# Performance work log

Measured on AMD Instinct MI355X. Metric: run time of the kernel, lower is better.

The kernel has to match this reference:

```python
import jax, jax.numpy as jnp
import numpy as np


def pairwise_euclidean_distance(x, y):
    # x: [N, D], y: [K, D] -> [N, K] squared Euclidean distances
    cross = -2.0 * (x @ y.T)
    x_term = jnp.sum(x * x, axis=1, keepdims=True)      # [N, 1]
    y_term = jnp.sum(y * y, axis=1, keepdims=True).T    # [1, K]
    return cross + x_term + y_term


def quantize(z, centroids):
    # z: [B, T, D], centroids: [K, D]
    B, T, D = z.shape
    flat = z.reshape(-1, D)                              # [N, D]
    distances = pairwise_euclidean_distance(flat, centroids)
    alignment = jnp.argmin(distances, axis=1)            # [N]
    q = centroids[alignment]                             # gather [N, D]
    # straight-through estimator: grad flows to z, not centroids
    q = flat + jax.lax.stop_gradient(q - flat)
    return q.reshape(B, T, D)


def setup_inputs() -> dict:
    key = jax.random.key(0)
    ks = jax.random.split(key, 5)
    B, T, F, D, K = 16, 2048, 80, 512, 2048
    return {
        "x": jax.random.normal(ks[0], (B, T, F), dtype=jnp.float32),
        "W_enc": jax.random.normal(ks[1], (F, D), dtype=jnp.float32) * (1.0 / np.sqrt(F)),
        "b_enc": jnp.zeros((D,), dtype=jnp.float32),
        "centroids": jax.random.normal(ks[2], (K, D), dtype=jnp.float32),
        "W_dec": jax.random.normal(ks[3], (D, F), dtype=jnp.float32) * (1.0 / np.sqrt(D)),
        "b_dec": jnp.zeros((F,), dtype=jnp.float32),
    }


def reference(x, W_enc, b_enc, centroids, W_dec, b_dec):
    z = x @ W_enc + b_enc            # encoder: [B, T, D]
    zq = quantize(z, centroids)      # VQ: distance + argmin + gather
    out = zq @ W_dec + b_dec         # decoder: [B, T, F]
    return out
```

## Files before the change

kernel.cpp:

```cpp
#include <hip/hip_runtime.h>
#include <hip/hip_bf16.h>

#define N_TOK  32768
#define F_IN   80
#define D_DIM  512
#define K_CENT 2048
#define F_OUT  80
#define TM     16
#define KP     96
#define M2     0.5f
#define QSLOTS 12
#define QREC   104
#define TREC   416
#define JTOT   160

typedef __attribute__((ext_vector_type(8)))  short bf16x8;
typedef __attribute__((ext_vector_type(4)))  float fx4;
typedef __attribute__((ext_vector_type(16))) float fx16;

#define AS3 __attribute__((address_space(3)))
#define AS1 __attribute__((address_space(1)))

__device__ inline unsigned short f2bf(float f) {
    unsigned u = __float_as_uint(f);
    return (unsigned short)((u + 0x7FFFu + ((u >> 16) & 1u)) >> 16);
}
__device__ inline float bf2f(unsigned short h) {
    return __uint_as_float((unsigned)h << 16);
}

__device__ inline void gll16(const unsigned short* g, unsigned short* l) {
    __builtin_amdgcn_global_load_lds((const AS1 unsigned*)g, (AS3 unsigned*)l, 16, 0, 0);
}

__device__ inline unsigned fkey(float f) {
    unsigned b = __float_as_uint(f);
    return b ^ ((b >> 31) ? 0xFFFFFFFFu : 0x80000000u);
}
__device__ inline float keyf(unsigned k) {
    unsigned b = k ^ ((k & 0x80000000u) ? 0x80000000u : 0xFFFFFFFFu);
    return __uint_as_float(b);
}

__device__ inline size_t frag32_addr(int row, int k) {
    int sub = (row >> 5) * 2 + ((k >> 4) & 1);
    int L = (row & 31) + ((k >> 3) & 1) * 32;
    return (size_t)sub * 512 + L * 8 + (k & 7);
}

__global__ __launch_bounds__(256) void k_prep1(
    const float* __restrict__ x, const float* __restrict__ Wenc,
    const float* __restrict__ Wdec,
    unsigned short* __restrict__ xbt, float* __restrict__ Bcat) {
    const int bid = blockIdx.x, tid = threadIdx.x;
    if (bid < 1536) {
        int o = bid * 256 + tid;
        int m = o / 12;
        int ko = (o - m * 12) * 8;
        unsigned short u[8];
        if (ko < F_IN) {
            const float* src = x + (size_t)m * F_IN + ko;
            float4 v0 = *(const float4*)src;
            float4 v1 = *(const float4*)(src + 4);
            u[0]=f2bf(v0.x); u[1]=f2bf(v0.y); u[2]=f2bf(v0.z); u[3]=f2bf(v0.w);
            u[4]=f2bf(v1.x); u[5]=f2bf(v1.y); u[6]=f2bf(v1.z); u[7]=f2bf(v1.w);
        } else if (ko == 80) {
            u[0] = 0x3F80; u[1] = 0x3F80;
#pragma unroll
            for (int j = 2; j < 8; ++j) u[j] = 0;
        } else {
#pragma unroll
            for (int j = 0; j < 8; ++j) u[j] = 0;
        }
        int mt = m >> 7, kt = ko >> 5, row = m & 127, kl = ko & 31;
        uint4 p;
        p.x = (unsigned)u[0] | ((unsigned)u[1] << 16);
        p.y = (unsigned)u[2] | ((unsigned)u[3] << 16);
        p.z = (unsigned)u[4] | ((unsigned)u[5] << 16);
        p.w = (unsigned)u[6] | ((unsigned)u[7] << 16);
        *(uint4*)&xbt[(size_t)(mt * 3 + kt) * 4096 + frag32_addr(row, kl)] = p;
    } else {
        int e = (bid - 1536) * 256 + tid;
        int d = e / JTOT, j = e - d * JTOT;
        float v = (j < F_OUT) ? Wdec[(size_t)d * F_OUT + j]
                              : Wenc[(size_t)(j - F_OUT) * D_DIM + d];
        Bcat[e] = v;
    }
}

__global__ void k_cadjf2(const float* __restrict__ cent, const float* __restrict__ benc,
                         float* __restrict__ cnorm, unsigned short* __restrict__ Gbt) {
    int wave = threadIdx.x >> 6, lane = threadIdx.x & 63;
    int k = blockIdx.x * 4 + wave;
    const float* row = cent + (size_t)k * D_DIM;
    float s = 0.f, t = 0.f;
#pragma unroll
    for (int j = 0; j < 8; ++j) {
        float c = row[lane + 64 * j];
        float b = benc[lane + 64 * j];
        s += c * c; t += b * c;
    }
#pragma unroll
    for (int off = 32; off; off >>= 1) { s += __shfl_down(s, off); t += __shfl_down(t, off); }
    const int nt = k >> 7, cl = k & 127;
    const size_t tb = (size_t)(nt * 3 + 2) * 4096;
    if (lane < 14)
        Gbt[tb + frag32_addr(cl, 18 + lane)] = 0;
    if (lane == 0) {
        cnorm[k] = s;
        float v = -0.5f * (s - 2.0f * t);
        unsigned short h = f2bf(v);
        unsigned short l = f2bf(v - bf2f(h));
        Gbt[tb + frag32_addr(cl, 16)] = h;
        Gbt[tb + frag32_addr(cl, 17)] = l;
    }
}

__global__ __launch_bounds__(192) void k_cgemm(
    const float* __restrict__ cent, const float* __restrict__ Bcat,
    const float* __restrict__ bdec, unsigned short* __restrict__ Gbt,
    float* __restrict__ dec) {
    const int j = threadIdx.x;
    if (j >= JTOT) return;
    const int k0 = blockIdx.x * 4;
    const float* c0 = cent + (size_t)k0 * D_DIM;
    float a0 = 0.f, a1 = 0.f, a2 = 0.f, a3 = 0.f;
#pragma unroll 4
    for (int d = 0; d < D_DIM; ++d) {
        float b  = Bcat[d * JTOT + j];
        float v0 = c0[d];
        float v1 = c0[D_DIM + d];
        float v2 = c0[2 * D_DIM + d];
        float v3 = c0[3 * D_DIM + d];
        a0 += v0 * b; a1 += v1 * b; a2 += v2 * b; a3 += v3 * b;
    }
    float a[4] = { a0, a1, a2, a3 };
    if (j < F_OUT) {
        float bd = bdec[j];
#pragma unroll
        for (int c = 0; c < 4; ++c)
            dec[(size_t)(k0 + c) * F_OUT + j] = a[c] + bd;
    } else {
        int f = j - F_OUT;
#pragma unroll
        for (int c = 0; c < 4; ++c) {
            int k = k0 + c;
            Gbt[(size_t)((k >> 7) * 3 + (f >> 5)) * 4096 + frag32_addr(k & 127, f & 31)]
                = f2bf(a[c]);
        }
    }
}

__global__ __launch_bounds__(512) void k_dist3(
    const unsigned short* __restrict__ xbt, const unsigned short* __restrict__ Gbt,
    char* __restrict__ lists) {
    __shared__ unsigned short Bs[2][12288];
    __shared__ int cnt[128];
    __shared__ unsigned mxk[128];

    const int tid = threadIdx.x;
    const int bid = blockIdx.x;
    const int mt = bid >> 2, nq = bid & 3;
    const int lane = tid & 63;
    const int wave = tid >> 6;
    const int tg = wave >> 1;
    const int ch = wave & 1;
    const int col = lane & 31;
    const int hi = lane >> 5;

    if (tid < 128) { cnt[tid] = 0; mxk[tid] = 0u; }

    bf16x8 bfr[6];
    const unsigned short* Ab = xbt + (size_t)mt * 12288;
#pragma unroll
    for (int kc = 0; kc < 6; ++kc)
        bfr[kc] = *(const bf16x8*)&Ab[(kc >> 1) * 4096 + (tg * 2 + (kc & 1)) * 512 + lane * 8];

    const int woff = (tid & ~63) * 8;
    const unsigned short* Gq = Gbt + (size_t)nq * 4 * 12288;
#pragma unroll
    for (int q = 0; q < 3; ++q)
        gll16(Gq + q * 4096 + tid * 8, &Bs[0][0] + q * 4096 + woff);

    float rmax = -3.4e38f;
    int cur = 0;
    for (int t4 = 0; t4 < 4; ++t4) {
        __syncthreads();
        if (t4 + 1 < 4) {
#pragma unroll
            for (int q = 0; q < 3; ++q)
                gll16(Gq + (size_t)(t4 + 1) * 12288 + q * 4096 + tid * 8,
                      &Bs[cur ^ 1][0] + q * 4096 + woff);
        }
        const unsigned short* B = &Bs[cur][0];
        fx16 acc[2];
#pragma unroll
        for (int u = 0; u < 2; ++u)
#pragma unroll
            for (int r = 0; r < 16; ++r) acc[u][r] = 0.f;
#pragma unroll
        for (int kc = 0; kc < 6; ++kc) {
#pragma unroll
            for (int u = 0; u < 2; ++u) {
                bf16x8 a = *(const bf16x8*)&B[(kc >> 1) * 4096
                             + ((ch * 2 + u) * 2 + (kc & 1)) * 512 + lane * 8];
                acc[u] = __builtin_amdgcn_mfma_f32_32x32x16_bf16(a, bfr[kc], acc[u], 0, 0, 0);
            }
        }
        float m = acc[0][0];
#pragma unroll
        for (int r = 1; r < 16; ++r) m = fmaxf(m, acc[0][r]);
#pragma unroll
        for (int r = 0; r < 16; ++r) m = fmaxf(m, acc[1][r]);
        m = fmaxf(m, __shfl_xor(m, 32));
        rmax = fmaxf(rmax, m);
        const float th = rmax - M2;
        const int tk = tg * 32 + col;
        char* qrec = lists + (size_t)(mt * 128 + tk) * TREC + nq * QREC;
#pragma unroll
        for (int u = 0; u < 2; ++u)
#pragma unroll
            for (int r = 0; r < 16; ++r) {
                float v = acc[u][r];
                if (v >= th) {
                    int slot = atomicAdd(&cnt[tk], 1);
                    if (slot < QSLOTS) {
                        uint2 e;
                        e.x = __float_as_uint(v);
                        e.y = (unsigned)((nq * 4 + t4) * 128 + (ch * 2 + u) * 32
                                         + (r & 3) + 8 * (r >> 2) + 4 * hi);
                        *(uint2*)(qrec + 8 + slot * 8) = e;
                    }
                }
            }
        cur ^= 1;
    }
    if (lane < 32) atomicMax(&mxk[tg * 32 + lane], fkey(rmax));
    __syncthreads();
    if (tid < 128) {
        uint2 h;
        h.x = (unsigned)cnt[tid];
        h.y = __float_as_uint(keyf(mxk[tid]));
        *(uint2*)(lists + (size_t)(mt * 128 + tid) * TREC + nq * QREC) = h;
    }
}

__global__ __launch_bounds__(256) void k_merge3(
    const char* __restrict__ lists, const float* __restrict__ cnorm,
    const float* __restrict__ cent, const float* __restrict__ x,
    const float* __restrict__ Wenc, const float* __restrict__ benc,
    const float* __restrict__ dec, float* __restrict__ out) {
    const int lane = threadIdx.x & 63;
    const int wid = blockIdx.x * 4 + (threadIdx.x >> 6);
    const int q = lane / 13, s = lane - q * 13;
    for (int it = 0; it < 4; ++it) {
        const int token = wid + it * 8192;
        const char* base = lists + (size_t)token * TREC;
        uint2 w = make_uint2(0u, 0u);
        if (lane < 52) w = *(const uint2*)(base + q * QREC + s * 8);
        const bool ishdr = (lane < 52) && (s == 0);
        float gm = ishdr ? __uint_as_float(w.y) : -3.4e38f;
#pragma unroll
        for (int off = 1; off < 64; off <<= 1) gm = fmaxf(gm, __shfl_xor(gm, off));
        const float th = gm - M2;
        unsigned long long anyovf = __ballot(ishdr && ((int)w.x > QSLOTS));
        int qcnt = __shfl((int)w.x, q * 13);
        int c12 = qcnt < QSLOTS ? qcnt : QSLOTS;
        bool cand = (lane < 52) && (s >= 1) && (s - 1 < c12) && (__uint_as_float(w.x) >= th);
        unsigned long long bal = __ballot(cand);
        int ns = __popcll(bal);
        int ans;
        if (!anyovf && ns == 1) {
            ans = __shfl((int)w.y, __ffsll(bal) - 1);
        } else {
            float z8[8];
#pragma unroll
            for (int j = 0; j < 8; ++j) z8[j] = benc[lane * 8 + j];
            const float* xr = x + (size_t)token * F_IN;
            const float* wp = Wenc + lane * 8;
            for (int f = 0; f < F_IN; ++f) {
                float xf = xr[f];
                fx4 w0 = *(const fx4*)(wp + (size_t)f * D_DIM);
                fx4 w1 = *(const fx4*)(wp + (size_t)f * D_DIM + 4);
                z8[0] += xf * w0.x; z8[1] += xf * w0.y; z8[2] += xf * w0.z; z8[3] += xf * w0.w;
                z8[4] += xf * w1.x; z8[5] += xf * w1.y; z8[6] += xf * w1.z; z8[7] += xf * w1.w;
            }
            float bd = 1e30f; int bn = 0x7FFFFFFF;
            if (!anyovf) {
                unsigned long long m = bal;
                while (m) {
                    int src = __ffsll(m) - 1; m &= m - 1;
                    int ci = __shfl((int)w.y, src);
                    const float* cr = cent + (size_t)ci * D_DIM + lane * 8;
                    fx4 c0 = *(const fx4*)cr, c1 = *(const fx4*)(cr + 4);
                    float dp = z8[0] * c0.x + z8[1] * c0.y + z8[2] * c0.z + z8[3] * c0.w
                             + z8[4] * c1.x + z8[5] * c1.y + z8[6] * c1.z + z8[7] * c1.w;
#pragma unroll
                    for (int off = 1; off < 64; off <<= 1) dp += __shfl_xor(dp, off);
                    float de = cnorm[ci] - 2.0f * dp;
                    if (de < bd || (de == bd && ci < bn)) { bd = de; bn = ci; }
                }
            } else {
                for (int ci = 0; ci < K_CENT; ++ci) {
                    const float* cr = cent + (size_t)ci * D_DIM + lane * 8;
                    fx4 c0 = *(const fx4*)cr, c1 = *(const fx4*)(cr + 4);
                    float dp = z8[0] * c0.x + z8[1] * c0.y + z8[2] * c0.z + z8[3] * c0.w
                             + z8[4] * c1.x + z8[5] * c1.y + z8[6] * c1.z + z8[7] * c1.w;
#pragma unroll
                    for (int off = 1; off < 64; off <<= 1) dp += __shfl_xor(dp, off);
                    float de = cnorm[ci] - 2.0f * dp;
                    if (de < bd || (de == bd && ci < bn)) { bd = de; bn = ci; }
                }
            }
            ans = bn;
        }
        const float* dr = dec + (size_t)ans * F_OUT;
        float* orow = out + (size_t)token * F_OUT;
        orow[lane] = dr[lane];
        if (lane < F_OUT - 64) orow[64 + lane] = dr[64 + lane];
    }
}

__global__ void k_transpose(const float* __restrict__ cent, float* __restrict__ centT) {
    __shared__ float tile[64][65];
    int kb = blockIdx.x * 64, db = blockIdx.y * 64;
    int lx = threadIdx.x & 63, ly = threadIdx.x >> 6;
#pragma unroll
    for (int i = 0; i < 16; ++i) {
        int row = ly + i * 4;
        tile[row][lx] = cent[(size_t)(kb + row) * D_DIM + db + lx];
    }
    __syncthreads();
#pragma unroll
    for (int i = 0; i < 16; ++i) {
        int row = ly + i * 4;
        centT[(size_t)(db + row) * K_CENT + kb + lx] = tile[lx][row];
    }
}

__global__ void k_cnorm(const float* __restrict__ cent, float* __restrict__ cnorm) {
    int wave = threadIdx.x >> 6, lane = threadIdx.x & 63;
    int k = blockIdx.x * 4 + wave;
    const float* row = cent + (size_t)k * D_DIM;
    float s = 0.f;
#pragma unroll
    for (int j = 0; j < 8; ++j) { float v = row[lane + 64 * j]; s += v * v; }
#pragma unroll
    for (int off = 32; off; off >>= 1) s += __shfl_down(s, off);
    if (lane == 0) cnorm[k] = s;
}

__global__ void k_dec(const float* __restrict__ cent, const float* __restrict__ Wdec,
                      const float* __restrict__ bdec, float* __restrict__ dec) {
    __shared__ float cs[D_DIM];
    int k = blockIdx.x;
    for (int d = threadIdx.x; d < D_DIM; d += blockDim.x) cs[d] = cent[(size_t)k * D_DIM + d];
    __syncthreads();
    int f = threadIdx.x;
    if (f < F_OUT) {
        float a0 = 0.f, a1 = 0.f, a2 = 0.f, a3 = 0.f;
#pragma unroll 4
        for (int d = 0; d < D_DIM; d += 4) {
            a0 += cs[d + 0] * Wdec[(d + 0) * F_OUT + f];
            a1 += cs[d + 1] * Wdec[(d + 1) * F_OUT + f];
            a2 += cs[d + 2] * Wdec[(d + 2) * F_OUT + f];
            a3 += cs[d + 3] * Wdec[(d + 3) * F_OUT + f];
        }
        dec[(size_t)k * F_OUT + f] = a0 + a1 + a2 + a3 + bdec[f];
    }
}

__global__ void k_out(const float* __restrict__ dec, const int* __restrict__ idx,
                      float* __restrict__ out) {
    int e0 = blockIdx.x * 2560;
#pragma unroll
    for (int r = 0; r < 10; ++r) {
        int e = e0 + threadIdx.x + r * 256;
        int n = e / F_OUT, f = e - n * F_OUT;
        out[e] = dec[(size_t)idx[n] * F_OUT + f];
    }
}

__global__ __launch_bounds__(256) void k_main(
    const float* __restrict__ x, const float* __restrict__ Wenc,
    const float* __restrict__ benc, const float* __restrict__ centT,
    const float* __restrict__ cnorm, int* __restrict__ idxOut) {
    __shared__ float xs[TM * F_IN];
    __shared__ float zs[TM][D_DIM];
    float* pv = &zs[0][0];
    int*   pi = (int*)(&zs[0][0] + 256 * TM);
    const int tid = threadIdx.x;
    const int tok0 = blockIdx.x * TM;
    for (int e = tid; e < TM * F_IN; e += 256) xs[e] = x[(size_t)tok0 * F_IN + e];
    __syncthreads();
    {
        float acc0[TM], acc1[TM];
#pragma unroll
        for (int t = 0; t < TM; ++t) { acc0[t] = 0.f; acc1[t] = 0.f; }
        const float2 b2 = ((const float2*)benc)[tid];
#pragma unroll 4
        for (int f4 = 0; f4 < F_IN; f4 += 4) {
            float2 w0 = ((const float2*)(Wenc + (size_t)(f4 + 0) * D_DIM))[tid];
            float2 w1 = ((const float2*)(Wenc + (size_t)(f4 + 1) * D_DIM))[tid];
            float2 w2 = ((const float2*)(Wenc + (size_t)(f4 + 2) * D_DIM))[tid];
            float2 w3 = ((const float2*)(Wenc + (size_t)(f4 + 3) * D_DIM))[tid];
#pragma unroll
            for (int t = 0; t < TM; ++t) {
                float4 xv = *(const float4*)&xs[t * F_IN + f4];
                acc0[t] += xv.x * w0.x + xv.y * w1.x + xv.z * w2.x + xv.w * w3.x;
                acc1[t] += xv.x * w0.y + xv.y * w1.y + xv.z * w2.y + xv.w * w3.y;
            }
        }
#pragma unroll
        for (int t = 0; t < TM; ++t)
            *(float2*)&zs[t][2 * tid] = make_float2(acc0[t] + b2.x, acc1[t] + b2.y);
    }
    __syncthreads();
    float minv[TM]; int mini[TM];
#pragma unroll
    for (int t = 0; t < TM; ++t) { minv[t] = 3.4e38f; mini[t] = 0; }
    for (int iter = 0; iter < 2; ++iter) {
        float acc[4][TM];
#pragma unroll
        for (int j = 0; j < 4; ++j)
#pragma unroll
            for (int t = 0; t < TM; ++t) acc[j][t] = 0.f;
        const int cbase = iter * 1024 + tid;
        for (int d4 = 0; d4 < D_DIM; d4 += 4) {
            float cv[4][4];
#pragma unroll
            for (int dd = 0; dd < 4; ++dd) {
                const float* cp = centT + (size_t)(d4 + dd) * K_CENT + cbase;
                cv[dd][0] = cp[0]; cv[dd][1] = cp[256]; cv[dd][2] = cp[512]; cv[dd][3] = cp[768];
            }
#pragma unroll
            for (int t = 0; t < TM; ++t) {
                float4 zv = *(const float4*)&zs[t][d4];
#pragma unroll
                for (int j = 0; j < 4; ++j)
                    acc[j][t] += zv.x * cv[0][j] + zv.y * cv[1][j] + zv.z * cv[2][j] + zv.w * cv[3][j];
            }
        }
#pragma unroll
        for (int j = 0; j < 4; ++j) {
            int c = cbase + j * 256;
            float cn = cnorm[c];
#pragma unroll
            for (int t = 0; t < TM; ++t) {
                float dist = cn - 2.f * acc[j][t];
                if (dist < minv[t]) { minv[t] = dist; mini[t] = c; }
            }
        }
    }
    __syncthreads();
#pragma unroll
    for (int t = 0; t < TM; ++t) { pv[tid * TM + t] = minv[t]; pi[tid * TM + t] = mini[t]; }
    __syncthreads();
    {
        int t = tid & 15, g = tid >> 4;
        float bv = 3.4e38f; int bi = 0x7fffffff;
        for (int j = 0; j < 16; ++j) {
            int r2 = g + 16 * j;
            float vv = pv[r2 * TM + t]; int i2 = pi[r2 * TM + t];
            if (vv < bv || (vv == bv && i2 < bi)) { bv = vv; bi = i2; }
        }
        pv[g * TM + t] = bv; pi[g * TM + t] = bi;
    }
    __syncthreads();
    if (tid < TM) {
        int t = tid;
        float bv = 3.4e38f; int bi = 0x7fffffff;
        for (int g = 0; g < 16; ++g) {
            float vv = pv[g * TM + t]; int i2 = pi[g * TM + t];
            if (vv < bv || (vv == bv && i2 < bi)) { bv = vv; bi = i2; }
        }
        idxOut[tok0 + t] = bi;
    }
}

extern "C" void kernel_launch(void* const* d_in, const int* in_sizes, int n_in,
                              void* d_out, int out_size, void* d_ws, size_t ws_size,
                              hipStream_t stream) {
    const float* x    = (const float*)d_in[0];
    const float* Wenc = (const float*)d_in[1];
    const float* benc = (const float*)d_in[2];
    const float* cent = (const float*)d_in[3];
    const float* Wdec = (const float*)d_in[4];
    const float* bdec = (const float*)d_in[5];
    float* out = (float*)d_out;

    const size_t L_B  = (size_t)N_TOK * TREC;
    const size_t XB_B = (size_t)N_TOK * KP * 2;
    const size_t GB_B = (size_t)K_CENT * KP * 2;
    const size_t N_B  = (size_t)K_CENT * 4;
    const size_t D_B  = (size_t)K_CENT * F_OUT * 4;
    const size_t BC_B = (size_t)D_DIM * JTOT * 4;
    const size_t NEED = L_B + XB_B + GB_B + N_B + D_B + BC_B;

    if (ws_size >= NEED) {
        char* w = (char*)d_ws;
        char*           lists = w;                            w += L_B;
        unsigned short* xbt   = (unsigned short*)w;           w += XB_B;
        unsigned short* Gbt   = (unsigned short*)w;           w += GB_B;
        float*          cnorm = (float*)w;                    w += N_B;
        float*          dec   = (float*)w;                    w += D_B;
        float*          Bcat  = (float*)w;

        k_prep1<<<1856, 256, 0, stream>>>(x, Wenc, Wdec, xbt, Bcat);
        k_cadjf2<<<K_CENT / 4, 256, 0, stream>>>(cent, benc, cnorm, Gbt);
        k_cgemm<<<K_CENT / 4, 192, 0, stream>>>(cent, Bcat, bdec, Gbt, dec);
        k_dist3<<<1024, 512, 0, stream>>>(xbt, Gbt, lists);
        k_merge3<<<2048, 256, 0, stream>>>(lists, cnorm, cent, x, Wenc, benc, dec, out);
    } else {
        float* centT = (float*)d_ws;
        float* cnorm = centT + (size_t)D_DIM * K_CENT;
        float* dec   = cnorm + K_CENT;
        int*   idx   = (int*)(dec + (size_t)K_CENT * F_OUT);
        k_transpose<<<dim3(K_CENT / 64, D_DIM / 64), 256, 0, stream>>>(cent, centT);
        k_cnorm<<<K_CENT / 4, 256, 0, stream>>>(cent, cnorm);
        k_dec<<<K_CENT, 128, 0, stream>>>(cent, Wdec, bdec, dec);
        k_main<<<N_TOK / TM, 256, 0, stream>>>(x, Wenc, benc, centT, cnorm, idx);
        k_out<<<N_TOK * F_OUT / 2560, 256, 0, stream>>>(dec, idx, out);
    }
}
```

Baseline: 112.8 us.

## Fuse centroid-norm kernel into prep and split cgemm reduction across two thread halves

The centroid norm and bias-adjust computation moves out of its own kernel and into the prep kernel as an extra range of blocks, which removes one launch. The centroid-side GEMM now uses 384 threads per block: each half handles half of the D dimension, and the two partial sums are combined through shared memory. This doubles the parallelism in a small, latency-bound precompute kernel, at the cost of a sync and a shared-memory reduction. These precompute stages are a small part of the total next to the distance kernel.

```diff
diff --git a/kernel.cpp b/kernel.cpp
--- a/kernel.cpp
+++ b/kernel.cpp
@@ -50,8 +50,10 @@
 
 __global__ __launch_bounds__(256) void k_prep1(
     const float* __restrict__ x, const float* __restrict__ Wenc,
-    const float* __restrict__ Wdec,
-    unsigned short* __restrict__ xbt, float* __restrict__ Bcat) {
+    const float* __restrict__ Wdec, const float* __restrict__ cent,
+    const float* __restrict__ benc,
+    unsigned short* __restrict__ xbt, float* __restrict__ Bcat,
+    float* __restrict__ cnorm, unsigned short* __restrict__ Gbt) {
     const int bid = blockIdx.x, tid = threadIdx.x;
     if (bid < 1536) {
         int o = bid * 256 + tid;
@@ -79,74 +81,80 @@
         p.z = (unsigned)u[4] | ((unsigned)u[5] << 16);
         p.w = (unsigned)u[6] | ((unsigned)u[7] << 16);
         *(uint4*)&xbt[(size_t)(mt * 3 + kt) * 4096 + frag32_addr(row, kl)] = p;
-    } else {
+    } else if (bid < 1856) {
         int e = (bid - 1536) * 256 + tid;
         int d = e / JTOT, j = e - d * JTOT;
         float v = (j < F_OUT) ? Wdec[(size_t)d * F_OUT + j]
                               : Wenc[(size_t)(j - F_OUT) * D_DIM + d];
         Bcat[e] = v;
-    }
-}
-
-__global__ void k_cadjf2(const float* __restrict__ cent, const float* __restrict__ benc,
-                         float* __restrict__ cnorm, unsigned short* __restrict__ Gbt) {
-    int wave = threadIdx.x >> 6, lane = threadIdx.x & 63;
-    int k = blockIdx.x * 4 + wave;
-    const float* row = cent + (size_t)k * D_DIM;
-    float s = 0.f, t = 0.f;
-#pragma unroll
-    for (int j = 0; j < 8; ++j) {
-        float c = row[lane + 64 * j];
-        float b = benc[lane + 64 * j];
-        s += c * c; t += b * c;
-    }
-#pragma unroll
-    for (int off = 32; off; off >>= 1) { s += __shfl_down(s, off); t += __shfl_down(t, off); }
-    const int nt = k >> 7, cl = k & 127;
-    const size_t tb = (size_t)(nt * 3 + 2) * 4096;
-    if (lane < 14)
-        Gbt[tb + frag32_addr(cl, 18 + lane)] = 0;
-    if (lane == 0) {
-        cnorm[k] = s;
-        float v = -0.5f * (s - 2.0f * t);
-        unsigned short h = f2bf(v);
-        unsigned short l = f2bf(v - bf2f(h));
-        Gbt[tb + frag32_addr(cl, 16)] = h;
-        Gbt[tb + frag32_addr(cl, 17)] = l;
-    }
-}
-
-__global__ __launch_bounds__(192) void k_cgemm(
+    } else {
+        int wave = tid >> 6, lane = tid & 63;
+        int k = (bid - 1856) * 4 + wave;
+        const float* row = cent + (size_t)k * D_DIM;
+        float s = 0.f, t = 0.f;
+#pragma unroll
+        for (int j = 0; j < 8; ++j) {
+            float c = row[lane + 64 * j];
+            float b = benc[lane + 64 * j];
+            s += c * c; t += b * c;
+        }
+#pragma unroll
+        for (int off = 32; off; off >>= 1) { s += __shfl_down(s, off); t += __shfl_down(t, off); }
+        const int nt = k >> 7, cl = k & 127;
+        const size_t tb = (size_t)(nt * 3 + 2) * 4096;
+        if (lane < 14)
+            Gbt[tb + frag32_addr(cl, 18 + lane)] = 0;
+        if (lane == 0) {
+            cnorm[k] = s;
+            float v = -0.5f * (s - 2.0f * t);
+            unsigned short h = f2bf(v);
+            unsigned short l = f2bf(v - bf2f(h));
+            Gbt[tb + frag32_addr(cl, 16)] = h;
+            Gbt[tb + frag32_addr(cl, 17)] = l;
+        }
+    }
+}
+
+__global__ __launch_bounds__(384) void k_cgemm2(
     const float* __restrict__ cent, const float* __restrict__ Bcat,
     const float* __restrict__ bdec, unsigned short* __restrict__ Gbt,
     float* __restrict__ dec) {
-    const int j = threadIdx.x;
-    if (j >= JTOT) return;
+    __shared__ float pacc[192][4];
+    const int tid = threadIdx.x;
+    const int j = tid % 192;
+    const int dh = tid / 192;
     const int k0 = blockIdx.x * 4;
-    const float* c0 = cent + (size_t)k0 * D_DIM;
     float a0 = 0.f, a1 = 0.f, a2 = 0.f, a3 = 0.f;
+    if (j < JTOT) {
+        const float* c0 = cent + (size_t)k0 * D_DIM + dh * 256;
+        const float* bp = Bcat + (size_t)dh * 256 * JTOT + j;
 #pragma unroll 4
-    for (int d = 0; d < D_DIM; ++d) {
-        float b  = Bcat[d * JTOT + j];
-        float v0 = c0[d];
-        float v1 = c0[D_DIM + d];
-        float v2 = c0[2 * D_DIM + d];
-        float v3 = c0[3 * D_DIM + d];
-        a0 += v0 * b; a1 += v1 * b; a2 += v2 * b; a3 += v3 * b;
-    }
-    float a[4] = { a0, a1, a2, a3 };
-    if (j < F_OUT) {
-        float bd = bdec[j];
-#pragma unroll
-        for (int c = 0; c < 4; ++c)
-            dec[(size_t)(k0 + c) * F_OUT + j] = a[c] + bd;
-    } else {
-        int f = j - F_OUT;
-#pragma unroll
-        for (int c = 0; c < 4; ++c) {
-            int k = k0 + c;
-            Gbt[(size_t)((k >> 7) * 3 + (f >> 5)) * 4096 + frag32_addr(k & 127, f & 31)]
-                = f2bf(a[c]);
+        for (int d = 0; d < 256; ++d) {
+            float b  = bp[d * JTOT];
+            a0 += c0[d] * b;
+            a1 += c0[D_DIM + d] * b;
+            a2 += c0[2 * D_DIM + d] * b;
+            a3 += c0[3 * D_DIM + d] * b;
+        }
+        if (dh == 1) { pacc[j][0] = a0; pacc[j][1] = a1; pacc[j][2] = a2; pacc[j][3] = a3; }
+    }
+    __syncthreads();
+    if (dh == 0 && j < JTOT) {
+        a0 += pacc[j][0]; a1 += pacc[j][1]; a2 += pacc[j][2]; a3 += pacc[j][3];
+        float a[4] = { a0, a1, a2, a3 };
+        if (j < F_OUT) {
+            float bd = bdec[j];
+#pragma unroll
+            for (int c = 0; c < 4; ++c)
+                dec[(size_t)(k0 + c) * F_OUT + j] = a[c] + bd;
+        } else {
+            int f = j - F_OUT;
+#pragma unroll
+            for (int c = 0; c < 4; ++c) {
+                int k = k0 + c;
+                Gbt[(size_t)((k >> 7) * 3 + (f >> 5)) * 4096 + frag32_addr(k & 127, f & 31)]
+                    = f2bf(a[c]);
+            }
         }
     }
 }
@@ -506,9 +514,9 @@
         float*          dec   = (float*)w;                    w += D_B;
         float*          Bcat  = (float*)w;
 
-        k_prep1<<<1856, 256, 0, stream>>>(x, Wenc, Wdec, xbt, Bcat);
-        k_cadjf2<<<K_CENT / 4, 256, 0, stream>>>(cent, benc, cnorm, Gbt);
-        k_cgemm<<<K_CENT / 4, 192, 0, stream>>>(cent, Bcat, bdec, Gbt, dec);
+        k_prep1<<<2368, 256, 0, stream>>>(x, Wenc, Wdec, cent, benc,
+                                          xbt, Bcat, cnorm, Gbt);
+        k_cgemm2<<<K_CENT / 4, 384, 0, stream>>>(cent, Bcat, bdec, Gbt, dec);
         k_dist3<<<1024, 512, 0, stream>>>(xbt, Gbt, lists);
         k_merge3<<<2048, 256, 0, stream>>>(lists, cnorm, cent, x, Wenc, benc, dec, out);
     } else {
```

New measurement: 102.3 us. 9.3% less time.
